# Optimization experiments

Measured on AMD Instinct MI355X. Metric: run time of the kernel, lower is better.

Reference implementation:

```python
import math
import jax, jax.numpy as jnp
import numpy as np

N, T, C, V = 16, 2048, 512, 500


def setup_inputs() -> dict:
    key = jax.random.key(0)
    k1, k2, k3 = jax.random.split(key, 3)
    x = jax.random.normal(k1, (N, T, C), dtype=jnp.float32)
    x_lens = jax.random.randint(k2, (N,), 1, T + 1).astype(jnp.int64)
    # stand-in for CTC log-posteriors; randn makes the blank channel pass the
    ctc_output = jax.random.normal(k3, (N, T, V), dtype=jnp.float32)
    return {"x": x, "x_lens": x_lens, "ctc_output": ctc_output, "blank_id": 0}


def reference(x, x_lens, ctc_output, blank_id):
    # x: [N, T, C], x_lens: [N], ctc_output: [N, T, V]
    n, t_max, _ = x.shape
    t = jnp.arange(t_max)
    padding_mask = t[None, :] >= x_lens[:, None]                      # [N, T]
    non_blank = (ctc_output[:, :, blank_id] < math.log(0.9)) & (~padding_mask)
    lens_fr = non_blank.sum(axis=1)                                   # [N]
    # stable argsort of ~mask: kept frame indices first, in original order
    order = jnp.argsort(~non_blank, axis=1, stable=True)              # [N, T]
    x_fr = jnp.take_along_axis(x, order[:, :, None], axis=1)          # [N, T, C]
    valid = t[None, :] < lens_fr[:, None]
    x_fr = jnp.where(valid[:, :, None], x_fr, jnp.zeros((), x.dtype))  # zero pad like pad_sequence
    t_prime = int(jnp.max(lens_fr))  # concrete (eager) -> [N, T', C] like torch
    return x_fr[:, :t_prime, :], lens_fr
```

## Files before the change

### kernel.cpp

```cpp
#include <hip/hip_runtime.h>
#include <hip/hip_bf16.h>


__global__ void mask_kernel(const float* __restrict__ ctc,
                            const void* __restrict__ x_lens_raw,
                            const int* __restrict__ blank_id_p,
                            int N, int T, int V,
                            unsigned long long* __restrict__ masks,
                            int* __restrict__ counts) {
    const int gidx = blockIdx.x * blockDim.x + threadIdx.x;
    const int lane = threadIdx.x & 63;
    const int NT = N * T;

    bool keep = false;
    if (gidx < NT) {
        int n = gidx / T;
        int t = gidx - n * T;
        const int* li = (const int*)x_lens_raw;
        long long L = (N > 1 && li[1] == 0) ? ((const long long*)x_lens_raw)[n]
                                            : (long long)li[n];
        float v = ctc[(long long)gidx * V + *blank_id_p];
        keep = (v < -0.10536052f) && ((long long)t < L);
    }
    unsigned long long bal = __ballot(keep);
    if (lane == 0 && gidx < NT) {
        masks[gidx >> 6] = bal;
        counts[gidx >> 6] = __popcll(bal);
    }
}

#define RPB 16

__global__ __launch_bounds__(256) void gather_kernel(
        const float* __restrict__ x,
        const unsigned long long* __restrict__ masks,
        const int* __restrict__ counts,
        float* __restrict__ out,
        float* __restrict__ lens_out,
        int Tp, int T) {
    const int C = 512;
    const int NCPS = T >> 6;
    const int n    = blockIdx.y;
    const int tid  = threadIdx.x;
    const int lane = tid & 63;
    const int sub  = tid >> 6;

    __shared__ int pfx[65];

    if (tid < 64) {
        int c = tid;
        int v = (c < NCPS) ? counts[n * NCPS + c] : 0;
        int incl = v;
        #pragma unroll
        for (int d = 1; d < 64; d <<= 1) {
            int o = __shfl_up(incl, d, 64);
            if (lane >= d) incl += o;
        }
        if (c < NCPS) pfx[c + 1] = incl;
        if (c == 0) pfx[0] = 0;
    }
    __syncthreads();
    const int lens = pfx[NCPS];
    if (blockIdx.x == 0 && tid == 0) lens_out[n] = (float)lens;

    for (int pass = 0; pass < RPB / 4; ++pass) {
        int p = blockIdx.x * RPB + pass * 4 + sub;
        if (p >= Tp) break;

        float4 a = make_float4(0.f, 0.f, 0.f, 0.f);
        float4 b = a;
        if (p < lens) {
            int lo = 0, hi = NCPS;
            while (hi - lo > 1) {
                int mid = (lo + hi) >> 1;
                if (pfx[mid] <= p) lo = mid; else hi = mid;
            }
            int r = p - pfx[lo];
            unsigned long long m = masks[n * NCPS + lo];
            int base = 0;
            #pragma unroll
            for (int w = 32; w >= 1; w >>= 1) {
                int cnt = __popcll(m & ((1ull << w) - 1ull));
                if (r >= cnt) { r -= cnt; m >>= w; base += w; }
            }
            int tsrc = (lo << 6) + base;
            const float4* src = (const float4*)(x + ((long long)n * T + tsrc) * C);
            a = src[lane * 2];
            b = src[lane * 2 + 1];
        }
        float4* dst = (float4*)(out + ((long long)n * Tp + p) * C);
        dst[lane * 2]     = a;
        dst[lane * 2 + 1] = b;
    }
}

extern "C" void kernel_launch(void* const* d_in, const int* in_sizes, int n_in,
                              void* d_out, int out_size, void* d_ws, size_t ws_size,
                              hipStream_t stream) {
    const float* x        = (const float*)d_in[0];
    const void*  x_lens   = d_in[1];
    const float* ctc      = (const float*)d_in[2];
    const int*   blank_id = (const int*)d_in[3];

    const int N = in_sizes[1];
    const int C = 512;
    const int V = 500;
    const int T = in_sizes[0] / (N * C);
    const int Tp = (out_size - N) / (N * C);
    const int NCPS = T >> 6;

    unsigned long long* masks = (unsigned long long*)d_ws;
    int* counts = (int*)(masks + (long long)N * NCPS);

    float* out      = (float*)d_out;
    float* lens_out = out + (long long)N * Tp * C;

    const int NT = N * T;
    mask_kernel<<<(NT + 255) / 256, 256, 0, stream>>>(ctc, x_lens, blank_id,
                                                      N, T, V, masks, counts);

    dim3 ggrid((Tp + RPB - 1) / RPB, N);
    gather_kernel<<<ggrid, 256, 0, stream>>>(x, masks, counts, out, lens_out, Tp, T);
}
```

Before: 19.54 us.

## Fuse mask computation into gather kernel with per-block redundant mask build

After: 19.57 us. About the same (+0.2%).

```diff
diff --git a/kernel.cpp b/kernel.cpp
--- a/kernel.cpp
+++ b/kernel.cpp
@@ -2,81 +2,76 @@
 #include <hip/hip_bf16.h>
 
 
-__global__ void mask_kernel(const float* __restrict__ ctc,
-                            const void* __restrict__ x_lens_raw,
-                            const int* __restrict__ blank_id_p,
-                            int N, int T, int V,
-                            unsigned long long* __restrict__ masks,
-                            int* __restrict__ counts) {
-    const int gidx = blockIdx.x * blockDim.x + threadIdx.x;
-    const int lane = threadIdx.x & 63;
-    const int NT = N * T;
-
-    bool keep = false;
-    if (gidx < NT) {
-        int n = gidx / T;
-        int t = gidx - n * T;
-        const int* li = (const int*)x_lens_raw;
-        long long L = (N > 1 && li[1] == 0) ? ((const long long*)x_lens_raw)[n]
-                                            : (long long)li[n];
-        float v = ctc[(long long)gidx * V + *blank_id_p];
-        keep = (v < -0.10536052f) && ((long long)t < L);
-    }
-    unsigned long long bal = __ballot(keep);
-    if (lane == 0 && gidx < NT) {
-        masks[gidx >> 6] = bal;
-        counts[gidx >> 6] = __popcll(bal);
-    }
-}
-
-#define RPB 16
-
-__global__ __launch_bounds__(256) void gather_kernel(
+__global__ __launch_bounds__(1024) void fused_kernel(
         const float* __restrict__ x,
-        const unsigned long long* __restrict__ masks,
-        const int* __restrict__ counts,
+        const void* __restrict__ x_lens_raw,
+        const float* __restrict__ ctc,
+        const int* __restrict__ blank_id_p,
+        int N, int T, int V, int Tp,
         float* __restrict__ out,
-        float* __restrict__ lens_out,
-        int Tp, int T) {
+        float* __restrict__ lens_out) {
     const int C = 512;
-    const int NCPS = T >> 6;
     const int n    = blockIdx.y;
     const int tid  = threadIdx.x;
     const int lane = tid & 63;
-    const int sub  = tid >> 6;
+    const int wid  = tid >> 6;
+    const int ITERS  = (T + 1023) >> 10;
+    const int NCHUNK = ITERS * 16;
 
+    __shared__ unsigned long long smask[64];
+    __shared__ int wcnt[64];
     __shared__ int pfx[65];
+
+    const int* li = (const int*)x_lens_raw;
+    long long L = (N > 1 && li[1] == 0) ? ((const long long*)x_lens_raw)[n]
+                                        : (long long)li[n];
+    const int blank = *blank_id_p;
+    const float thr = -0.10536052f;
+
+    for (int j = 0; j < ITERS; ++j) {
+        int t = (j << 10) + tid;
+        bool keep = false;
+        if (t < T) {
+            float v = ctc[((long long)n * T + t) * V + blank];
+            keep = (v < thr) && ((long long)t < L);
+        }
+        unsigned long long bal = __ballot(keep);
+        if (lane == 0) {
+            smask[j * 16 + wid] = bal;
+            wcnt[j * 16 + wid]  = __popcll(bal);
+        }
+    }
+    __syncthreads();
 
     if (tid < 64) {
         int c = tid;
-        int v = (c < NCPS) ? counts[n * NCPS + c] : 0;
-        int incl = v;
+        int incl = (c < NCHUNK) ? wcnt[c] : 0;
         #pragma unroll
         for (int d = 1; d < 64; d <<= 1) {
             int o = __shfl_up(incl, d, 64);
             if (lane >= d) incl += o;
         }
-        if (c < NCPS) pfx[c + 1] = incl;
+        if (c < NCHUNK) pfx[c + 1] = incl;
         if (c == 0) pfx[0] = 0;
     }
     __syncthreads();
-    const int lens = pfx[NCPS];
+    const int lens = pfx[NCHUNK];
     if (blockIdx.x == 0 && tid == 0) lens_out[n] = (float)lens;
 
-    for (int pass = 0; pass < RPB / 4; ++pass) {
-        int p = blockIdx.x * RPB + pass * 4 + sub;
+    for (int pass = 0; pass < 4; ++pass) {
+        int p = blockIdx.x * 64 + pass * 16 + wid;
         if (p >= Tp) break;
 
         float4 a = make_float4(0.f, 0.f, 0.f, 0.f);
         float4 b = a;
         if (p < lens) {
-            int lo = 0, hi = NCPS;
+            int lo = 0, hi = NCHUNK;
             while (hi - lo > 1) {
                 int mid = (lo + hi) >> 1;
                 if (pfx[mid] <= p) lo = mid; else hi = mid;
             }
             int r = p - pfx[lo];
-            unsigned long long m = masks[n * NCPS + lo];
+            unsigned long long m = smask[lo];
             int base = 0;
             #pragma unroll
             for (int w = 32; w >= 1; w >>= 1) {
@@ -107,18 +102,11 @@
     const int V = 500;
     const int T = in_sizes[0] / (N * C);
     const int Tp = (out_size - N) / (N * C);
-    const int NCPS = T >> 6;
-
-    unsigned long long* masks = (unsigned long long*)d_ws;
-    int* counts = (int*)(masks + (long long)N * NCPS);
 
     float* out      = (float*)d_out;
     float* lens_out = out + (long long)N * Tp * C;
 
-    const int NT = N * T;
-    mask_kernel<<<(NT + 255) / 256, 256, 0, stream>>>(ctc, x_lens, blank_id,
-                                                      N, T, V, masks, counts);
-
-    dim3 ggrid((Tp + RPB - 1) / RPB, N);
-    gather_kernel<<<ggrid, 256, 0, stream>>>(x, masks, counts, out, lens_out, Tp, T);
+    dim3 grid((Tp + 63) / 64, N);
+    fused_kernel<<<grid, 1024, 0, stream>>>(x, x_lens, ctc, blank_id,
+                                            N, T, V, Tp, out, lens_out);
 }
```
